# Optimization experiments

Hardware: AMD Instinct MI355X
Metric: run time of the kernel (lower is better)

The kernel has to match this reference:

```python
import jax, jax.numpy as jnp
import numpy as np

N_NODES = 100000
N_EDGES = 1600000
IN_C, HID, N_CLS = 128, 128, 40


def setup_inputs() -> dict:
    key = jax.random.key(0)
    ks = jax.random.split(key, 8)
    x = jax.random.normal(ks[0], (N_NODES, IN_C), dtype=jnp.float32)
    edge_index = jax.random.randint(ks[1], (2, N_EDGES), 0, N_NODES, dtype=jnp.int64)
    s1 = 1.0 / np.sqrt(IN_C)
    s2 = 1.0 / np.sqrt(HID)
    return {
        "x": x,
        "edge_index": edge_index,
        "Wl1": jax.random.normal(ks[2], (IN_C, HID), dtype=jnp.float32) * s1,
        "Wr1": jax.random.normal(ks[3], (IN_C, HID), dtype=jnp.float32) * s1,
        "b1": jnp.zeros((HID,), dtype=jnp.float32),
        "Wl2": jax.random.normal(ks[4], (HID, N_CLS), dtype=jnp.float32) * s2,
        "Wr2": jax.random.normal(ks[5], (HID, N_CLS), dtype=jnp.float32) * s2,
        "b2": jnp.zeros((N_CLS,), dtype=jnp.float32),
    }


def _sage_conv(x, src, dst, Wl, Wr, b):
    # mean-aggregate neighbor features at destination nodes
    n = x.shape[0]
    agg = jax.ops.segment_sum(x[src], dst, num_segments=n)           # [N, C]
    cnt = jax.ops.segment_sum(jnp.ones((src.shape[0],), x.dtype), dst, num_segments=n)
    mean = agg / jnp.maximum(cnt, 1.0)[:, None]
    return mean @ Wl + x @ Wr + b


def reference(x, edge_index, Wl1, Wr1, b1, Wl2, Wr2, b2):
    src, dst = edge_index[0], edge_index[1]
    h = jax.nn.relu(_sage_conv(x, src, dst, Wl1, Wr1, b1))
    return _sage_conv(h, src, dst, Wl2, Wr2, b2)
```

## Files before the change

kernel.cpp:

```cpp
#include <hip/hip_runtime.h>

#define C_IN 128
#define N_CLS 40
#define ZB   40

#define NPB   256
#define MAXNB 512
#define CAP   6144
#define BCSTR 16
#define BINB  8192

typedef __attribute__((ext_vector_type(8))) short bf16x8;
typedef __attribute__((ext_vector_type(4))) float f32x4;
typedef __attribute__((ext_vector_type(2))) float f32x2;

__device__ __forceinline__ ushort f2b(float f) {
  union { float f; unsigned u; } v; v.f = f;
  unsigned r = v.u + 0x7FFF + ((v.u >> 16) & 1);
  return (ushort)(r >> 16);
}
__device__ __forceinline__ float b2f(ushort u) {
  union { unsigned u; float f; } v; v.u = ((unsigned)u) << 16;
  return v.f;
}
__device__ __forceinline__ unsigned packbf(float lo, float hi) {
  return (unsigned)f2b(lo) | ((unsigned)f2b(hi) << 16);
}
__device__ __forceinline__ void acc2(float& fa, float& fb, unsigned u) {
  union { unsigned u; float f; } lo, hi;
  lo.u = u << 16; hi.u = u & 0xFFFF0000u;
  fa += lo.f; fb += hi.f;
}

#if __has_builtin(__builtin_amdgcn_cvt_pk_f32_fp8) && __has_builtin(__builtin_amdgcn_cvt_pk_fp8_f32)
#define HW_FP8 1
#else
#define HW_FP8 0
#endif

__device__ __forceinline__ float f8dec1(unsigned b) {
  unsigned E = (b >> 3) & 15, M = b & 7;
  if (E) {
    union { unsigned u; float f; } v;
    v.u = ((b & 0x80u) << 24) | ((E + 120u) << 23) | (M << 20);
    return v.f;
  }
  float m = (float)(int)M * 0.001953125f;
  return (b & 0x80u) ? -m : m;
}
__device__ __forceinline__ unsigned f8enc1(float x) {
  union { float f; unsigned u; } v; v.f = x;
  unsigned s = (v.u >> 31) << 7;
  float ax = fabsf(x);
  if (ax < 9.765625e-4f) return s;
  if (ax < 0.015625f) {
    int M = (int)rintf(ax * 512.0f);
    return (M >= 8) ? (s | 0x08u) : (s | (unsigned)M);
  }
  if (ax > 448.0f) return s | 0x7Eu;
  unsigned au = v.u & 0x7FFFFFFFu;
  unsigned r = au + 0x7FFFFu + ((au >> 20) & 1);
  int e = (int)(r >> 23) - 127;
  unsigned M = (r >> 20) & 7;
  if (e > 8) return s | 0x7Eu;
  return s | ((unsigned)(e + 7) << 3) | M;
}
__device__ __forceinline__ void accf8x4(float* a, unsigned u) {
#if HW_FP8
  f32x2 lo = __builtin_amdgcn_cvt_pk_f32_fp8((int)u, false);
  f32x2 hi = __builtin_amdgcn_cvt_pk_f32_fp8((int)u, true);
  a[0] += lo[0]; a[1] += lo[1]; a[2] += hi[0]; a[3] += hi[1];
#else
  a[0] += f8dec1(u & 0xFF); a[1] += f8dec1((u >> 8) & 0xFF);
  a[2] += f8dec1((u >> 16) & 0xFF); a[3] += f8dec1(u >> 24);
#endif
}
__device__ __forceinline__ unsigned packf8x4(float x0, float x1, float x2, float x3) {
#if HW_FP8
  int p = 0;
  p = __builtin_amdgcn_cvt_pk_fp8_f32(x0, x1, p, false);
  p = __builtin_amdgcn_cvt_pk_fp8_f32(x2, x3, p, true);
  return (unsigned)p;
#else
  return f8enc1(x0) | (f8enc1(x1) << 8) | (f8enc1(x2) << 16) | (f8enc1(x3) << 24);
#endif
}
__device__ __forceinline__ unsigned char f8enc_byte(float x) {
#if HW_FP8
  return (unsigned char)(__builtin_amdgcn_cvt_pk_fp8_f32(x, x, 0, false) & 0xFF);
#else
  return (unsigned char)f8enc1(x);
#endif
}

__global__ __launch_bounds__(256) void bin_cvt_kernel(
    const int* __restrict__ src, const int* __restrict__ dst,
    int* __restrict__ bcur, unsigned* __restrict__ staged, int E, int NB, int nbin,
    const float* __restrict__ xin, ushort* __restrict__ xb,
    unsigned char* __restrict__ xf8, long n8)
{
  __shared__ unsigned sw[BINB];
  __shared__ ushort  sb[BINB];
  __shared__ int cnt[MAXNB];
  __shared__ int base[MAXNB];
  const int tid = threadIdx.x;
  if (blockIdx.x >= nbin) {
    long i = ((long)(blockIdx.x - nbin) * 256 + tid);
    if (i < n8) {
      const float4 a = *reinterpret_cast<const float4*>(xin + i * 8);
      const float4 b = *reinterpret_cast<const float4*>(xin + i * 8 + 4);
      uint4 o;
      o.x = packbf(a.x, a.y);
      o.y = packbf(a.z, a.w);
      o.z = packbf(b.x, b.y);
      o.w = packbf(b.z, b.w);
      *reinterpret_cast<uint4*>(xb + i * 8) = o;
      uint2 p;
      p.x = packf8x4(a.x, a.y, a.z, a.w);
      p.y = packf8x4(b.x, b.y, b.z, b.w);
      *reinterpret_cast<uint2*>(xf8 + i * 8) = p;
    }
    return;
  }
  for (int i = tid; i < NB; i += 256) cnt[i] = 0;
  __syncthreads();
  const int e0 = blockIdx.x * BINB;
  const int nE = min(BINB, E - e0);
  for (int k = tid; k < nE; k += 256) {
    int d = dst[e0 + k];
    int s = src[e0 + k];
    int b = d >> 8;
    sw[k] = (unsigned)s | ((unsigned)(d & 255) << 20);
    sb[k] = (ushort)b;
    atomicAdd(&cnt[b], 1);
  }
  __syncthreads();
  for (int i = tid; i < NB; i += 256) {
    int c = cnt[i];
    base[i] = (c > 0) ? atomicAdd(&bcur[i * BCSTR], c) : 0;
    cnt[i] = 0;
  }
  __syncthreads();
  for (int k = tid; k < nE; k += 256) {
    int b = sb[k];
    int pos = base[b] + atomicAdd(&cnt[b], 1);
    if (pos < CAP)
      staged[(size_t)b * CAP + pos] = sw[k];
  }
}

__global__ __launch_bounds__(256) void csr_kernel(
    const unsigned* __restrict__ staged, const int* __restrict__ bcur,
    int* __restrict__ row_ptr, int* __restrict__ deg, int* __restrict__ csr_src, int N)
{
  __shared__ unsigned st[CAP];
  __shared__ int dcnt[NPB];
  __shared__ int cur[NPB];
  __shared__ int wsum[4];
  __shared__ int rb_s;
  const int b = blockIdx.x, tid = threadIdx.x;
  const int cb = min(bcur[b * BCSTR], CAP);
  for (int i = tid; i < cb; i += 256) st[i] = staged[(size_t)b * CAP + i];
  int part = 0;
  for (int i = tid; i < b; i += 256) part += min(bcur[i * BCSTR], CAP);
  if (tid == 0) rb_s = 0;
  dcnt[tid] = 0;
  __syncthreads();
  #pragma unroll
  for (int off = 32; off > 0; off >>= 1) part += __shfl_down(part, off);
  if ((tid & 63) == 0 && part != 0) atomicAdd(&rb_s, part);
  for (int i = tid; i < cb; i += 256) atomicAdd(&dcnt[st[i] >> 20], 1);
  __syncthreads();
  const int rb = rb_s;
  int d = dcnt[tid];
  const int lane = tid & 63, w = tid >> 6;
  int inc = d;
  #pragma unroll
  for (int off = 1; off < 64; off <<= 1) {
    int v = __shfl_up(inc, off);
    if (lane >= off) inc += v;
  }
  if (lane == 63) wsum[w] = inc;
  __syncthreads();
  int wo = 0;
  for (int i = 0; i < w; ++i) wo += wsum[i];
  const int excl = wo + inc - d;
  cur[tid] = excl;
  const int node = b * NPB + tid;
  if (node < N) { row_ptr[node] = rb + excl; deg[node] = d; }
  __syncthreads();
  for (int i = tid; i < cb; i += 256) {
    unsigned wv = st[i];
    int p = atomicAdd(&cur[wv >> 20], 1);
    csr_src[rb + p] = (int)(wv & 0xFFFFF);
  }
}

__global__ __launch_bounds__(256) void agg1_ugemm_kernel(
    const unsigned char* __restrict__ xf8, const ushort* __restrict__ xb,
    const int* __restrict__ csr_src, const int* __restrict__ row_ptr,
    const int* __restrict__ deg, ushort* __restrict__ mean, int N, int nagg,
    const float* __restrict__ Wr, const float* __restrict__ bias,
    ushort* __restrict__ u, int ntiles, int ngem)
{
  __shared__ ushort sB[4 * 8 * 64 * 8];
  const int tid = threadIdx.x;
  if (blockIdx.x >= nagg) {
    for (int idx = tid; idx < 4 * 8 * 64; idx += 256) {
      int l  = idx & 63;
      int cg = (idx >> 6) & 7;
      int ks = idx >> 9;
      int c  = cg * 16 + (l & 15);
      int kb = ks * 32 + 8 * (l >> 4);
      ushort* p = &sB[idx * 8];
      #pragma unroll
      for (int j = 0; j < 8; ++j) p[j] = f2b(Wr[(kb + j) * C_IN + c]);
    }
    __syncthreads();
    const int w = tid >> 6, l = tid & 63;
    const int kg = l >> 4;
    for (int tile = blockIdx.x - nagg; tile < ntiles; tile += ngem) {
      int n0 = tile * 128 + w * 32;
      int rc0 = n0 + (l & 15);      rc0 = (rc0 < N) ? rc0 : (N - 1);
      int rc1 = n0 + 16 + (l & 15); rc1 = (rc1 < N) ? rc1 : (N - 1);
      f32x4 acc[2][8] = {};
      #pragma unroll
      for (int ks = 0; ks < 4; ++ks) {
        int kb = ks * 32 + kg * 8;
        bf16x8 a0 = *reinterpret_cast<const bf16x8*>(xb + (size_t)rc0 * C_IN + kb);
        bf16x8 a1 = *reinterpret_cast<const bf16x8*>(xb + (size_t)rc1 * C_IN + kb);
        #pragma unroll
        for (int cg = 0; cg < 8; ++cg) {
          bf16x8 b = *reinterpret_cast<const bf16x8*>(&sB[((ks * 8 + cg) * 64 + l) * 8]);
          acc[0][cg] = __builtin_amdgcn_mfma_f32_16x16x32_bf16(a0, b, acc[0][cg], 0, 0, 0);
          acc[1][cg] = __builtin_amdgcn_mfma_f32_16x16x32_bf16(a1, b, acc[1][cg], 0, 0, 0);
        }
      }
      const int rowoff = (l >> 4) * 4, colbase = l & 15;
      #pragma unroll
      for (int f = 0; f < 2; ++f) {
        #pragma unroll
        for (int cg = 0; cg < 8; ++cg) {
          int c = cg * 16 + colbase;
          float bc = bias[c];
          #pragma unroll
          for (int r = 0; r < 4; ++r) {
            int row = n0 + f * 16 + rowoff + r;
            if (row < N) u[(size_t)row * C_IN + c] = f2b(acc[f][cg][r] + bc);
          }
        }
      }
    }
    return;
  }
  int t = blockIdx.x * 256 + tid;
  int n = t >> 3;
  if (n >= N) return;
  int q = t & 7;
  int base = row_ptr[n];
  int d = deg[n];
  float a[16];
  #pragma unroll
  for (int i = 0; i < 16; ++i) a[i] = 0.f;
  if (d > 8) {
    const unsigned char* fq = xf8 + q * 16;
    int j = 0;
    for (; j + 4 <= d; j += 4) {
      int s0 = csr_src[base + j + 0];
      int s1 = csr_src[base + j + 1];
      int s2 = csr_src[base + j + 2];
      int s3 = csr_src[base + j + 3];
      uint4 v0 = *reinterpret_cast<const uint4*>(fq + (size_t)s0 * C_IN);
      uint4 v1 = *reinterpret_cast<const uint4*>(fq + (size_t)s1 * C_IN);
      uint4 v2 = *reinterpret_cast<const uint4*>(fq + (size_t)s2 * C_IN);
      uint4 v3 = *reinterpret_cast<const uint4*>(fq + (size_t)s3 * C_IN);
      accf8x4(a+0, v0.x); accf8x4(a+4, v0.y); accf8x4(a+8, v0.z); accf8x4(a+12, v0.w);
      accf8x4(a+0, v1.x); accf8x4(a+4, v1.y); accf8x4(a+8, v1.z); accf8x4(a+12, v1.w);
      accf8x4(a+0, v2.x); accf8x4(a+4, v2.y); accf8x4(a+8, v2.z); accf8x4(a+12, v2.w);
      accf8x4(a+0, v3.x); accf8x4(a+4, v3.y); accf8x4(a+8, v3.z); accf8x4(a+12, v3.w);
    }
    for (; j < d; ++j) {
      int s = csr_src[base + j];
      uint4 v = *reinterpret_cast<const uint4*>(fq + (size_t)s * C_IN);
      accf8x4(a+0, v.x); accf8x4(a+4, v.y); accf8x4(a+8, v.z); accf8x4(a+12, v.w);
    }
  } else {
    const ushort* fq = xb + q * 16;
    for (int j = 0; j < d; ++j) {
      int s = csr_src[base + j];
      uint4 w0 = *reinterpret_cast<const uint4*>(fq + (size_t)s * C_IN);
      uint4 w1 = *reinterpret_cast<const uint4*>(fq + (size_t)s * C_IN + 8);
      acc2(a[0],a[1],w0.x); acc2(a[2],a[3],w0.y); acc2(a[4],a[5],w0.z); acc2(a[6],a[7],w0.w);
      acc2(a[8],a[9],w1.x); acc2(a[10],a[11],w1.y); acc2(a[12],a[13],w1.z); acc2(a[14],a[15],w1.w);
    }
  }
  float inv = (d > 0) ? (1.0f / (float)d) : 0.0f;
  uint4 o0, o1;
  o0.x = packbf(a[0]*inv, a[1]*inv);  o0.y = packbf(a[2]*inv, a[3]*inv);
  o0.z = packbf(a[4]*inv, a[5]*inv);  o0.w = packbf(a[6]*inv, a[7]*inv);
  o1.x = packbf(a[8]*inv, a[9]*inv);  o1.y = packbf(a[10]*inv, a[11]*inv);
  o1.z = packbf(a[12]*inv, a[13]*inv); o1.w = packbf(a[14]*inv, a[15]*inv);
  uint4* mp = reinterpret_cast<uint4*>(mean + (size_t)n * C_IN + q * 16);
  mp[0] = o0;
  mp[1] = o1;
}

__global__ __launch_bounds__(256) void layer1b_mfma(
    const ushort* __restrict__ mb, const ushort* __restrict__ u,
    const float* __restrict__ Wl, ushort* __restrict__ h, int N, int ntiles)
{
  __shared__ ushort sB[4 * 8 * 64 * 8];
  const int tid = threadIdx.x;
  for (int idx = tid; idx < 4 * 8 * 64; idx += 256) {
    int l  = idx & 63;
    int cg = (idx >> 6) & 7;
    int ks = idx >> 9;
    int c  = cg * 16 + (l & 15);
    int kb = ks * 32 + 8 * (l >> 4);
    ushort* p = &sB[idx * 8];
    #pragma unroll
    for (int j = 0; j < 8; ++j) p[j] = f2b(Wl[(kb + j) * C_IN + c]);
  }
  __syncthreads();
  const int w = tid >> 6, l = tid & 63;
  const int kg = l >> 4;
  const int rowoff = (l >> 4) * 4, colbase = l & 15;
  for (int tile = blockIdx.x; tile < ntiles; tile += gridDim.x) {
    int n0 = tile * 128 + w * 32;
    int rc0 = n0 + (l & 15);      rc0 = (rc0 < N) ? rc0 : (N - 1);
    int rc1 = n0 + 16 + (l & 15); rc1 = (rc1 < N) ? rc1 : (N - 1);
    f32x4 acc[2][8];
    #pragma unroll
    for (int f = 0; f < 2; ++f) {
      #pragma unroll
      for (int cg = 0; cg < 8; ++cg) {
        int c = cg * 16 + colbase;
        #pragma unroll
        for (int r = 0; r < 4; ++r) {
          int row = n0 + f * 16 + rowoff + r;
          row = (row < N) ? row : (N - 1);
          acc[f][cg][r] = b2f(u[(size_t)row * C_IN + c]);
        }
      }
    }
    #pragma unroll
    for (int ks = 0; ks < 4; ++ks) {
      int kb = ks * 32 + kg * 8;
      bf16x8 a0 = *reinterpret_cast<const bf16x8*>(mb + (size_t)rc0 * C_IN + kb);
      bf16x8 a1 = *reinterpret_cast<const bf16x8*>(mb + (size_t)rc1 * C_IN + kb);
      #pragma unroll
      for (int cg = 0; cg < 8; ++cg) {
        bf16x8 b = *reinterpret_cast<const bf16x8*>(&sB[((ks * 8 + cg) * 64 + l) * 8]);
        acc[0][cg] = __builtin_amdgcn_mfma_f32_16x16x32_bf16(a0, b, acc[0][cg], 0, 0, 0);
        acc[1][cg] = __builtin_amdgcn_mfma_f32_16x16x32_bf16(a1, b, acc[1][cg], 0, 0, 0);
      }
    }
    #pragma unroll
    for (int f = 0; f < 2; ++f) {
      #pragma unroll
      for (int cg = 0; cg < 8; ++cg) {
        int c = cg * 16 + colbase;
        #pragma unroll
        for (int r = 0; r < 4; ++r) {
          int row = n0 + f * 16 + rowoff + r;
          if (row < N)
            h[(size_t)row * C_IN + c] = f2b(fmaxf(acc[f][cg][r], 0.0f));
        }
      }
    }
  }
}

__global__ __launch_bounds__(256) void gemm2_dual(
    const ushort* __restrict__ hb,
    const float* __restrict__ Wl, const float* __restrict__ Wr,
    unsigned char* __restrict__ z, float* __restrict__ out, int N, int ntiles)
{
  __shared__ ushort sBl[4 * 3 * 64 * 8];
  __shared__ ushort sBr[4 * 3 * 64 * 8];
  const int tid = threadIdx.x;
  for (int idx = tid; idx < 4 * 3 * 64; idx += 256) {
    int l  = idx & 63;
    int cg = (idx >> 6) % 3;
    int ks = idx / (3 * 64);
    int c  = cg * 16 + (l & 15);
    int kb = ks * 32 + 8 * (l >> 4);
    ushort* pl = &sBl[idx * 8];
    ushort* pr = &sBr[idx * 8];
    #pragma unroll
    for (int j = 0; j < 8; ++j) {
      int k = kb + j;
      float wl = 0.0f, wr = 0.0f;
      if (c < N_CLS) { wl = Wl[k * N_CLS + c]; wr = Wr[k * N_CLS + c]; }
      pl[j] = f2b(wl);
      pr[j] = f2b(wr);
    }
  }
  __syncthreads();
  const int w = tid >> 6, l = tid & 63;
  const int rfrag = l & 15, kg = l >> 4;
  for (int tile = blockIdx.x; tile < ntiles; tile += gridDim.x) {
    int n0 = tile * 128 + w * 32;
    int rc0 = n0 + rfrag;      rc0 = (rc0 < N) ? rc0 : (N - 1);
    int rc1 = n0 + 16 + rfrag; rc1 = (rc1 < N) ? rc1 : (N - 1);
    f32x4 az[2][3] = {};
    f32x4 ay[2][3] = {};
    #pragma unroll
    for (int ks = 0; ks < 4; ++ks) {
      int kb = ks * 32 + kg * 8;
      bf16x8 a0 = *reinterpret_cast<const bf16x8*>(hb + (size_t)rc0 * C_IN + kb);
      bf16x8 a1 = *reinterpret_cast<const bf16x8*>(hb + (size_t)rc1 * C_IN + kb);
      #pragma unroll
      for (int cg = 0; cg < 3; ++cg) {
        bf16x8 bl = *reinterpret_cast<const bf16x8*>(&sBl[((ks * 3 + cg) * 64 + l) * 8]);
        bf16x8 br = *reinterpret_cast<const bf16x8*>(&sBr[((ks * 3 + cg) * 64 + l) * 8]);
        az[0][cg] = __builtin_amdgcn_mfma_f32_16x16x32_bf16(a0, bl, az[0][cg], 0, 0, 0);
        az[1][cg] = __builtin_amdgcn_mfma_f32_16x16x32_bf16(a1, bl, az[1][cg], 0, 0, 0);
        ay[0][cg] = __builtin_amdgcn_mfma_f32_16x16x32_bf16(a0, br, ay[0][cg], 0, 0, 0);
        ay[1][cg] = __builtin_amdgcn_mfma_f32_16x16x32_bf16(a1, br, ay[1][cg], 0, 0, 0);
      }
    }
    const int rowoff = (l >> 4) * 4, colbase = l & 15;
    #pragma unroll
    for (int f = 0; f < 2; ++f) {
      #pragma unroll
      for (int cg = 0; cg < 3; ++cg) {
        int c = cg * 16 + colbase;
        if (c < N_CLS) {
          #pragma unroll
          for (int r = 0; r < 4; ++r) {
            int row = n0 + f * 16 + rowoff + r;
            if (row < N) {
              z[(size_t)row * ZB + c] = f8enc_byte(az[f][cg][r]);
              out[(size_t)row * N_CLS + c] = ay[f][cg][r];
            }
          }
        }
      }
    }
  }
}

__global__ __launch_bounds__(256) void agg2z_kernel(
    const unsigned char* __restrict__ z, const int* __restrict__ csr_src,
    const int* __restrict__ row_ptr, const int* __restrict__ deg,
    const float* __restrict__ b2, float* __restrict__ out, int N)
{
  unsigned w = blockIdx.x * 256 + threadIdx.x;
  unsigned n = w / 5u;
  if (n >= (unsigned)N) return;
  unsigned q = w - n * 5u;
  const unsigned char* zq = z + q * 8;
  int base = row_ptr[n];
  int d = deg[n];
  float a[8];
  #pragma unroll
  for (int i = 0; i < 8; ++i) a[i] = 0.f;
  int j = 0;
  for (; j + 4 <= d; j += 4) {
    int s0 = csr_src[base + j + 0];
    int s1 = csr_src[base + j + 1];
    int s2 = csr_src[base + j + 2];
    int s3 = csr_src[base + j + 3];
    uint2 v0 = *reinterpret_cast<const uint2*>(zq + (size_t)s0 * ZB);
    uint2 v1 = *reinterpret_cast<const uint2*>(zq + (size_t)s1 * ZB);
    uint2 v2 = *reinterpret_cast<const uint2*>(zq + (size_t)s2 * ZB);
    uint2 v3 = *reinterpret_cast<const uint2*>(zq + (size_t)s3 * ZB);
    accf8x4(a+0, v0.x); accf8x4(a+4, v0.y);
    accf8x4(a+0, v1.x); accf8x4(a+4, v1.y);
    accf8x4(a+0, v2.x); accf8x4(a+4, v2.y);
    accf8x4(a+0, v3.x); accf8x4(a+4, v3.y);
  }
  for (; j < d; ++j) {
    int s = csr_src[base + j];
    uint2 v = *reinterpret_cast<const uint2*>(zq + (size_t)s * ZB);
    accf8x4(a+0, v.x); accf8x4(a+4, v.y);
  }
  float inv = (d > 0) ? (1.0f / (float)d) : 0.0f;
  float* op = out + (size_t)n * N_CLS + q * 8;
  const float4 bA = *reinterpret_cast<const float4*>(b2 + q * 8);
  const float4 bB = *reinterpret_cast<const float4*>(b2 + q * 8 + 4);
  float4 y0 = *reinterpret_cast<const float4*>(op);
  float4 y1 = *reinterpret_cast<const float4*>(op + 4);
  y0.x += a[0] * inv + bA.x; y0.y += a[1] * inv + bA.y;
  y0.z += a[2] * inv + bA.z; y0.w += a[3] * inv + bA.w;
  y1.x += a[4] * inv + bB.x; y1.y += a[5] * inv + bB.y;
  y1.z += a[6] * inv + bB.z; y1.w += a[7] * inv + bB.w;
  *reinterpret_cast<float4*>(op) = y0;
  *reinterpret_cast<float4*>(op + 4) = y1;
}

extern "C" void kernel_launch(void* const* d_in, const int* in_sizes, int n_in,
                              void* d_out, int out_size, void* d_ws, size_t ws_size,
                              hipStream_t stream)
{
  const float* x   = (const float*)d_in[0];
  const int*   ei  = (const int*)d_in[1];
  const float* Wl1 = (const float*)d_in[2];
  const float* Wr1 = (const float*)d_in[3];
  const float* b1  = (const float*)d_in[4];
  const float* Wl2 = (const float*)d_in[5];
  const float* Wr2 = (const float*)d_in[6];
  const float* b2  = (const float*)d_in[7];
  float* out = (float*)d_out;

  const int N = in_sizes[0] / C_IN;
  const int E = in_sizes[1] / 2;
  const int* src = ei;
  const int* dst = ei + E;
  const int NB = (N + NPB - 1) / NPB;

  size_t Np = ((size_t)N + 255) & ~(size_t)255;
  size_t Ep = ((size_t)E + 255) & ~(size_t)255;
  int* wsi     = (int*)d_ws;
  int* bcur    = wsi;
  int* row_ptr = wsi + (size_t)MAXNB * BCSTR;
  int* deg     = row_ptr + Np;
  int* csr_src = deg + Np;
  unsigned* staged = (unsigned*)(csr_src + Ep);
  unsigned char* zb = (unsigned char*)staged;
  ushort* xb    = (ushort*)(staged + (size_t)MAXNB * CAP);
  ushort* meanb = xb + (size_t)N * C_IN;
  ushort* hb    = meanb + (size_t)N * C_IN;
  ushort* ub    = hb + (size_t)N * C_IN;
  unsigned char* xf8 = (unsigned char*)(ub + (size_t)N * C_IN);

  hipMemsetAsync(bcur, 0, (size_t)MAXNB * BCSTR * sizeof(int), stream);

  const int nbin = (E + BINB - 1) / BINB;
  long n8 = (long)N * C_IN / 8;
  const int ncvt = (int)((n8 + 255) / 256);
  bin_cvt_kernel<<<nbin + ncvt, 256, 0, stream>>>(src, dst, bcur, staged, E, NB, nbin,
                                                  x, xb, xf8, n8);

  csr_kernel<<<NB, 256, 0, stream>>>(staged, bcur, row_ptr, deg, csr_src, N);

  const int ntiles = (N + 127) / 128;
  const int nagg = (N * 8 + 255) / 256;
  const int ngem = 512;

  agg1_ugemm_kernel<<<nagg + ngem, 256, 0, stream>>>(xf8, xb, csr_src, row_ptr, deg,
                                                     meanb, N, nagg,
                                                     Wr1, b1, ub, ntiles, ngem);
  layer1b_mfma<<<512, 256, 0, stream>>>(meanb, ub, Wl1, hb, N, ntiles);

  gemm2_dual<<<512, 256, 0, stream>>>(hb, Wl2, Wr2, zb, out, N, ntiles);
  agg2z_kernel<<<(N * 5 + 255) / 256, 256, 0, stream>>>(zb, csr_src, row_ptr, deg, b2, out, N);
}
```

Before: 196.2 us.

## Move x@Wr1 GEMM into the binning/convert kernel, reading fp32 x directly

The root-side GEMM (x @ Wr1 + b1) moves out of the aggregation kernel and into the first binning/conversion kernel as extra blocks. Those blocks read fp32 x and convert it to bf16 in registers, so they no longer depend on the converted copy. The goal is to overlap the GEMM with edge binning, which is atomic-heavy and latency-bound, and to shorten the aggregation launch. Shared memory is overlapped through a union. The GEMM blocks now read twice as many bytes of x as before.

```diff
diff --git a/kernel.cpp b/kernel.cpp
--- a/kernel.cpp
+++ b/kernel.cpp
@@ -30,6 +30,14 @@
   union { unsigned u; float f; } lo, hi;
   lo.u = u << 16; hi.u = u & 0xFFFF0000u;
   fa += lo.f; fb += hi.f;
+}
+__device__ __forceinline__ bf16x8 ldfrag_f32(const float* p) {
+  float4 a = *reinterpret_cast<const float4*>(p);
+  float4 b = *reinterpret_cast<const float4*>(p + 4);
+  union { unsigned u[4]; bf16x8 v; } r;
+  r.u[0] = packbf(a.x, a.y); r.u[1] = packbf(a.z, a.w);
+  r.u[2] = packbf(b.x, b.y); r.u[3] = packbf(b.z, b.w);
+  return r.v;
 }
 
 #if __has_builtin(__builtin_amdgcn_cvt_pk_f32_fp8) && __has_builtin(__builtin_amdgcn_cvt_pk_fp8_f32)
@@ -93,17 +101,70 @@
 #endif
 }
 
-__global__ __launch_bounds__(256) void bin_cvt_kernel(
+union SharedP1 {
+  struct { unsigned sw[BINB]; ushort sb[BINB]; int cnt[MAXNB]; int base[MAXNB]; } b;
+  ushort gW[4 * 8 * 64 * 8];
+};
+
+__global__ __launch_bounds__(256) void bin_cvt_ugemm_kernel(
     const int* __restrict__ src, const int* __restrict__ dst,
-    int* __restrict__ bcur, unsigned* __restrict__ staged, int E, int NB, int nbin,
+    int* __restrict__ bcur, unsigned* __restrict__ staged, int E, int NB,
+    int nbin, int ncvt,
     const float* __restrict__ xin, ushort* __restrict__ xb,
-    unsigned char* __restrict__ xf8, long n8)
-{
-  __shared__ unsigned sw[BINB];
-  __shared__ ushort  sb[BINB];
-  __shared__ int cnt[MAXNB];
-  __shared__ int base[MAXNB];
+    unsigned char* __restrict__ xf8, long n8,
+    const float* __restrict__ Wr, const float* __restrict__ bias,
+    ushort* __restrict__ u, int N, int ntiles, int ngem)
+{
+  __shared__ SharedP1 sh;
   const int tid = threadIdx.x;
+  if (blockIdx.x >= nbin + ncvt) {
+    for (int idx = tid; idx < 4 * 8 * 64; idx += 256) {
+      int l  = idx & 63;
+      int cg = (idx >> 6) & 7;
+      int ks = idx >> 9;
+      int c  = cg * 16 + (l & 15);
+      int kb = ks * 32 + 8 * (l >> 4);
+      ushort* p = &sh.gW[idx * 8];
+      #pragma unroll
+      for (int j = 0; j < 8; ++j) p[j] = f2b(Wr[(kb + j) * C_IN + c]);
+    }
+    __syncthreads();
+    const int w = tid >> 6, l = tid & 63;
+    const int kg = l >> 4;
+    for (int tile = blockIdx.x - nbin - ncvt; tile < ntiles; tile += ngem) {
+      int n0 = tile * 128 + w * 32;
+      int rc0 = n0 + (l & 15);      rc0 = (rc0 < N) ? rc0 : (N - 1);
+      int rc1 = n0 + 16 + (l & 15); rc1 = (rc1 < N) ? rc1 : (N - 1);
+      f32x4 acc[2][8] = {};
+      #pragma unroll
+      for (int ks = 0; ks < 4; ++ks) {
+        int kb = ks * 32 + kg * 8;
+        bf16x8 a0 = ldfrag_f32(xin + (size_t)rc0 * C_IN + kb);
+        bf16x8 a1 = ldfrag_f32(xin + (size_t)rc1 * C_IN + kb);
+        #pragma unroll
+        for (int cg = 0; cg < 8; ++cg) {
+          bf16x8 b = *reinterpret_cast<const bf16x8*>(&sh.gW[((ks * 8 + cg) * 64 + l) * 8]);
+          acc[0][cg] = __builtin_amdgcn_mfma_f32_16x16x32_bf16(a0, b, acc[0][cg], 0, 0, 0);
+          acc[1][cg] = __builtin_amdgcn_mfma_f32_16x16x32_bf16(a1, b, acc[1][cg], 0, 0, 0);
+        }
+      }
+      const int rowoff = (l >> 4) * 4, colbase = l & 15;
+      #pragma unroll
+      for (int f = 0; f < 2; ++f) {
+        #pragma unroll
+        for (int cg = 0; cg < 8; ++cg) {
+          int c = cg * 16 + colbase;
+          float bc = bias[c];
+          #pragma unroll
+          for (int r = 0; r < 4; ++r) {
+            int row = n0 + f * 16 + rowoff + r;
+            if (row < N) u[(size_t)row * C_IN + c] = f2b(acc[f][cg][r] + bc);
+          }
+        }
+      }
+    }
+    return;
+  }
   if (blockIdx.x >= nbin) {
     long i = ((long)(blockIdx.x - nbin) * 256 + tid);
     if (i < n8) {
@@ -122,7 +183,7 @@
     }
     return;
   }
-  for (int i = tid; i < NB; i += 256) cnt[i] = 0;
+  for (int i = tid; i < NB; i += 256) sh.b.cnt[i] = 0;
   __syncthreads();
   const int e0 = blockIdx.x * BINB;
   const int nE = min(BINB, E - e0);
@@ -130,22 +191,22 @@
     int d = dst[e0 + k];
     int s = src[e0 + k];
     int b = d >> 8;
-    sw[k] = (unsigned)s | ((unsigned)(d & 255) << 20);
-    sb[k] = (ushort)b;
-    atomicAdd(&cnt[b], 1);
+    sh.b.sw[k] = (unsigned)s | ((unsigned)(d & 255) << 20);
+    sh.b.sb[k] = (ushort)b;
+    atomicAdd(&sh.b.cnt[b], 1);
   }
   __syncthreads();
   for (int i = tid; i < NB; i += 256) {
-    int c = cnt[i];
-    base[i] = (c > 0) ? atomicAdd(&bcur[i * BCSTR], c) : 0;
-    cnt[i] = 0;
+    int c = sh.b.cnt[i];
+    sh.b.base[i] = (c > 0) ? atomicAdd(&bcur[i * BCSTR], c) : 0;
+    sh.b.cnt[i] = 0;
   }
   __syncthreads();
   for (int k = tid; k < nE; k += 256) {
-    int b = sb[k];
-    int pos = base[b] + atomicAdd(&cnt[b], 1);
+    int b = sh.b.sb[k];
+    int pos = sh.b.base[b] + atomicAdd(&sh.b.cnt[b], 1);
     if (pos < CAP)
-      staged[(size_t)b * CAP + pos] = sw[k];
+      staged[(size_t)b * CAP + pos] = sh.b.sw[k];
   }
 }
 
@@ -196,64 +257,12 @@
   }
 }
 
-__global__ __launch_bounds__(256) void agg1_ugemm_kernel(
+__global__ __launch_bounds__(256) void agg1_kernel(
     const unsigned char* __restrict__ xf8, const ushort* __restrict__ xb,
     const int* __restrict__ csr_src, const int* __restrict__ row_ptr,
-    const int* __restrict__ deg, ushort* __restrict__ mean, int N, int nagg,
-    const float* __restrict__ Wr, const float* __restrict__ bias,
-    ushort* __restrict__ u, int ntiles, int ngem)
-{
-  __shared__ ushort sB[4 * 8 * 64 * 8];
-  const int tid = threadIdx.x;
-  if (blockIdx.x >= nagg) {
-    for (int idx = tid; idx < 4 * 8 * 64; idx += 256) {
-      int l  = idx & 63;
-      int cg = (idx >> 6) & 7;
-      int ks = idx >> 9;
-      int c  = cg * 16 + (l & 15);
-      int kb = ks * 32 + 8 * (l >> 4);
-      ushort* p = &sB[idx * 8];
-      #pragma unroll
-      for (int j = 0; j < 8; ++j) p[j] = f2b(Wr[(kb + j) * C_IN + c]);
-    }
-    __syncthreads();
-    const int w = tid >> 6, l = tid & 63;
-    const int kg = l >> 4;
-    for (int tile = blockIdx.x - nagg; tile < ntiles; tile += ngem) {
-      int n0 = tile * 128 + w * 32;
-      int rc0 = n0 + (l & 15);      rc0 = (rc0 < N) ? rc0 : (N - 1);
-      int rc1 = n0 + 16 + (l & 15); rc1 = (rc1 < N) ? rc1 : (N - 1);
-      f32x4 acc[2][8] = {};
-      #pragma unroll
-      for (int ks = 0; ks < 4; ++ks) {
-        int kb = ks * 32 + kg * 8;
-        bf16x8 a0 = *reinterpret_cast<const bf16x8*>(xb + (size_t)rc0 * C_IN + kb);
-        bf16x8 a1 = *reinterpret_cast<const bf16x8*>(xb + (size_t)rc1 * C_IN + kb);
-        #pragma unroll
-        for (int cg = 0; cg < 8; ++cg) {
-          bf16x8 b = *reinterpret_cast<const bf16x8*>(&sB[((ks * 8 + cg) * 64 + l) * 8]);
-          acc[0][cg] = __builtin_amdgcn_mfma_f32_16x16x32_bf16(a0, b, acc[0][cg], 0, 0, 0);
-          acc[1][cg] = __builtin_amdgcn_mfma_f32_16x16x32_bf16(a1, b, acc[1][cg], 0, 0, 0);
-        }
-      }
-      const int rowoff = (l >> 4) * 4, colbase = l & 15;
-      #pragma unroll
-      for (int f = 0; f < 2; ++f) {
-        #pragma unroll
-        for (int cg = 0; cg < 8; ++cg) {
-          int c = cg * 16 + colbase;
-          float bc = bias[c];
-          #pragma unroll
-          for (int r = 0; r < 4; ++r) {
-            int row = n0 + f * 16 + rowoff + r;
-            if (row < N) u[(size_t)row * C_IN + c] = f2b(acc[f][cg][r] + bc);
-          }
-        }
-      }
-    }
-    return;
-  }
-  int t = blockIdx.x * 256 + tid;
+    const int* __restrict__ deg, ushort* __restrict__ mean, int N)
+{
+  int t = blockIdx.x * 256 + threadIdx.x;
   int n = t >> 3;
   if (n >= N) return;
   int q = t & 7;
@@ -527,21 +536,19 @@
 
   hipMemsetAsync(bcur, 0, (size_t)MAXNB * BCSTR * sizeof(int), stream);
 
+  const int ntiles = (N + 127) / 128;
+  const int ngem = 512;
+
   const int nbin = (E + BINB - 1) / BINB;
   long n8 = (long)N * C_IN / 8;
   const int ncvt = (int)((n8 + 255) / 256);
-  bin_cvt_kernel<<<nbin + ncvt, 256, 0, stream>>>(src, dst, bcur, staged, E, NB, nbin,
-                                                  x, xb, xf8, n8);
+  bin_cvt_ugemm_kernel<<<nbin + ncvt + ngem, 256, 0, stream>>>(
+      src, dst, bcur, staged, E, NB, nbin, ncvt,
+      x, xb, xf8, n8, Wr1, b1, ub, N, ntiles, ngem);
 
   csr_kernel<<<NB, 256, 0, stream>>>(staged, bcur, row_ptr, deg, csr_src, N);
 
-  const int ntiles = (N + 127) / 128;
-  const int nagg = (N * 8 + 255) / 256;
-  const int ngem = 512;
-
-  agg1_ugemm_kernel<<<nagg + ngem, 256, 0, stream>>>(xf8, xb, csr_src, row_ptr, deg,
-                                                     meanb, N, nagg,
-                                                     Wr1, b1, ub, ntiles, ngem);
+  agg1_kernel<<<(N * 8 + 255) / 256, 256, 0, stream>>>(xf8, xb, csr_src, row_ptr, deg, meanb, N);
   layer1b_mfma<<<512, 256, 0, stream>>>(meanb, ub, Wl1, hb, N, ntiles);
 
   gemm2_dual<<<512, 256, 0, stream>>>(hb, Wl2, Wr2, zb, out, N, ntiles);
```

Measured after the change: 194.3 us. About the same (-1.0%).
